# Optimization experiments

Hardware: AMD Instinct MI355X
Metric: run time of the kernel (lower is better)

Reference implementation:

```python
import jax, jax.numpy as jnp
import numpy as np

B, M, E, H, TOPK = 1024, 10000, 8, 512, 2


def setup_inputs() -> dict:
    key = jax.random.key(0)
    ks = jax.random.split(key, 6)
    s_in = 1.0 / np.sqrt(M)
    s_h = 1.0 / np.sqrt(H)
    x = jax.random.normal(ks[0], (B, M), dtype=jnp.float32)
    # Expert params, torch Linear layout stacked over experts
    W1 = jax.random.uniform(ks[1], (E, H, M), jnp.float32, -s_in, s_in)
    b1 = jax.random.uniform(ks[2], (E, H), jnp.float32, -s_in, s_in)
    W2 = jax.random.uniform(ks[3], (E, M, H), jnp.float32, -s_h, s_h)
    b2 = jax.random.uniform(ks[4], (E, M), jnp.float32, -s_h, s_h)
    Wr = jax.random.uniform(ks[5], (E, M), jnp.float32, -s_in, s_in)  # router, no bias
    return {"x": x, "W1": W1, "b1": b1, "W2": W2, "b2": b2, "Wr": Wr}


def reference(x, W1, b1, W2, b2, Wr):
    # Router: logits [B, E], sparse top-k softmax weights scattered to dense [B, E]
    logits = jnp.einsum('bm,em->be', x, Wr)
    topk_vals, topk_idx = jax.lax.top_k(logits, TOPK)
    probs = jax.nn.softmax(topk_vals, axis=-1)
    rw = jnp.zeros_like(logits).at[jnp.arange(B)[:, None], topk_idx].set(probs)
    # Dense all-expert MLP (faithful to original: every expert runs on every token)
    h = jax.nn.relu(jnp.einsum('bm,ehm->beh', x, W1) + b1)      # [B, E, H]
    eo = jnp.einsum('beh,emh->bem', h, W2) + b2                  # [B, E, M]
    # Masked weighted combine
    out = jnp.sum(rw[:, :, None] * eo, axis=1)                   # [B, M]
    return out
```

## Files before the change

### kernel.cpp

```cpp
#include <hip/hip_runtime.h>
#include <hip/hip_bf16.h>


#define B_TOK 1024
#define M_DIM 10000
#define E_NUM 8
#define H_DIM 512
#define NSTEP 313

typedef __attribute__((ext_vector_type(4))) float fx4;
typedef __attribute__((ext_vector_type(8))) short sx8;
typedef __attribute__((ext_vector_type(4))) short sx4;

#define LSTR 40

__device__ __forceinline__ short f2bf(float f) {
  union { __hip_bfloat16 h; short s; } u;
  u.h = __float2bfloat16(f);
  return u.s;
}

__device__ __forceinline__ sx8 pack8(fx4 a, fx4 b) {
  sx8 r;
  r[0] = f2bf(a[0]); r[1] = f2bf(a[1]); r[2] = f2bf(a[2]); r[3] = f2bf(a[3]);
  r[4] = f2bf(b[0]); r[5] = f2bf(b[1]); r[6] = f2bf(b[2]); r[7] = f2bf(b[3]);
  return r;
}

__global__ void k_zero(int* cnt, int* cnt2) {
  if (threadIdx.x < E_NUM) cnt[threadIdx.x] = 0;
  if (threadIdx.x < 2 * E_NUM) cnt2[threadIdx.x] = 0;
}

__global__ __launch_bounds__(256) void k_router(
    const float* __restrict__ x, const float* __restrict__ Wr,
    int* __restrict__ cnt, int* __restrict__ cnt2,
    int* __restrict__ tokAll, int* __restrict__ qlist2, float* __restrict__ wlist2)
{
  int b = blockIdx.x, t = threadIdx.x;
  const float* xr = x + (size_t)b * M_DIM;
  double acc[E_NUM];
#pragma unroll
  for (int e = 0; e < E_NUM; e++) acc[e] = 0.0;
  for (int m = t; m < M_DIM; m += 256) {
    float xv = xr[m];
#pragma unroll
    for (int e = 0; e < E_NUM; e++)
      acc[e] += (double)xv * (double)Wr[e * M_DIM + m];
  }
#pragma unroll
  for (int e = 0; e < E_NUM; e++) {
#pragma unroll
    for (int off = 32; off > 0; off >>= 1)
      acc[e] += __shfl_xor(acc[e], off);
  }
  __shared__ double part[4][E_NUM];
  int wave = t >> 6;
  if ((t & 63) == 0) {
    for (int e = 0; e < E_NUM; e++) part[wave][e] = acc[e];
  }
  __syncthreads();
  if (t == 0) {
    double lg[E_NUM];
    for (int e = 0; e < E_NUM; e++)
      lg[e] = part[0][e] + part[1][e] + part[2][e] + part[3][e];
    int i0 = 0;
    for (int e = 1; e < E_NUM; e++) if (lg[e] > lg[i0]) i0 = e;
    int i1 = (i0 == 0) ? 1 : 0;
    for (int e = 0; e < E_NUM; e++) if (e != i0 && lg[e] > lg[i1]) i1 = e;
    double ex = exp(lg[i1] - lg[i0]);
    float p0 = (float)(1.0 / (1.0 + ex));
    float p1 = (float)(ex / (1.0 + ex));
    int q0 = atomicAdd(&cnt[i0], 1);
    tokAll[i0 * B_TOK + q0] = b;
    int j0 = atomicAdd(&cnt2[i0 * 2 + 0], 1);
    qlist2[(i0 * 2 + 0) * B_TOK + j0] = q0;
    wlist2[(i0 * 2 + 0) * B_TOK + j0] = p0;
    int q1 = atomicAdd(&cnt[i1], 1);
    tokAll[i1 * B_TOK + q1] = b;
    int j1 = atomicAdd(&cnt2[i1 * 2 + 1], 1);
    qlist2[(i1 * 2 + 1) * B_TOK + j1] = q1;
    wlist2[(i1 * 2 + 1) * B_TOK + j1] = p1;
  }
}

__global__ __launch_bounds__(256) void k_mlp1(
    const float* __restrict__ x, const float* __restrict__ W1,
    const int* __restrict__ cnt, const int* __restrict__ tokAll,
    float* __restrict__ partials, int CH)
{
  int e = blockIdx.z;
  int tt = blockIdx.y >> 2, nt = blockIdx.y & 3;
  int kc = blockIdx.x;

  __shared__ int sh_ne, sh_eoff;
  __shared__ __align__(16) short As[128 * LSTR];
  __shared__ __align__(16) short Bs[128 * LSTR];
  __shared__ int toks[128];

  int t = threadIdx.x;
  if (t == 0) {
    int off = 0;
    for (int k = 0; k < e; k++) off += cnt[k];
    sh_eoff = off; sh_ne = cnt[e];
  }
  __syncthreads();
  int ne = sh_ne, eoff = sh_eoff, row0 = tt * 128;
  if (row0 >= ne) return;
  int nvalid = min(128, ne - row0);

  if (t < 128) toks[t] = tokAll[e * B_TOK + row0 + min(t, nvalid - 1)];
  __syncthreads();

  int r4 = t >> 2, kch = t & 3;
  const float* xr0 = x + (size_t)toks[r4] * M_DIM + kch * 8;
  const float* xr1 = x + (size_t)toks[r4 + 64] * M_DIM + kch * 8;
  const float* wr0 = W1 + ((size_t)e * H_DIM + nt * 128 + r4) * M_DIM + kch * 8;
  const float* wr1 = W1 + ((size_t)e * H_DIM + nt * 128 + r4 + 64) * M_DIM + kch * 8;

  int lane = t & 63, wave = t >> 6;
  int wr = wave >> 1, wc = wave & 1;
  int lrow = lane & 15, khalf = lane >> 4;

  fx4 z4 = {0.f, 0.f, 0.f, 0.f};
  fx4 acc[4][4];
#pragma unroll
  for (int m = 0; m < 4; m++)
#pragma unroll
    for (int n = 0; n < 4; n++) acc[m][n] = z4;

  int s0 = kc * CH, s1 = min(s0 + CH, NSTEP);
  sx8 zv = {0, 0, 0, 0, 0, 0, 0, 0};

  sx8 a0, a1, b0, b1v;
  {
    int k0 = s0 * 32 + kch * 8;
    bool ok = (k0 + 8 <= M_DIM);
    a0  = ok ? pack8(*(const fx4*)(xr0 + s0 * 32), *(const fx4*)(xr0 + s0 * 32 + 4)) : zv;
    a1  = ok ? pack8(*(const fx4*)(xr1 + s0 * 32), *(const fx4*)(xr1 + s0 * 32 + 4)) : zv;
    b0  = ok ? pack8(*(const fx4*)(wr0 + s0 * 32), *(const fx4*)(wr0 + s0 * 32 + 4)) : zv;
    b1v = ok ? pack8(*(const fx4*)(wr1 + s0 * 32), *(const fx4*)(wr1 + s0 * 32 + 4)) : zv;
  }

  for (int s = s0; s < s1; s++) {
    __syncthreads();
    *(sx8*)(&As[r4 * LSTR + kch * 8]) = a0;
    *(sx8*)(&As[(r4 + 64) * LSTR + kch * 8]) = a1;
    *(sx8*)(&Bs[r4 * LSTR + kch * 8]) = b0;
    *(sx8*)(&Bs[(r4 + 64) * LSTR + kch * 8]) = b1v;
    __syncthreads();
    if (s + 1 < s1) {
      int kn = (s + 1) * 32;
      bool ok = (kn + kch * 8 + 8 <= M_DIM);
      a0  = ok ? pack8(*(const fx4*)(xr0 + kn), *(const fx4*)(xr0 + kn + 4)) : zv;
      a1  = ok ? pack8(*(const fx4*)(xr1 + kn), *(const fx4*)(xr1 + kn + 4)) : zv;
      b0  = ok ? pack8(*(const fx4*)(wr0 + kn), *(const fx4*)(wr0 + kn + 4)) : zv;
      b1v = ok ? pack8(*(const fx4*)(wr1 + kn), *(const fx4*)(wr1 + kn + 4)) : zv;
    }
    sx8 af[4], bf[4];
#pragma unroll
    for (int m = 0; m < 4; m++)
      af[m] = *(const sx8*)(&As[(wr * 64 + m * 16 + lrow) * LSTR + khalf * 8]);
#pragma unroll
    for (int n = 0; n < 4; n++)
      bf[n] = *(const sx8*)(&Bs[(wc * 64 + n * 16 + lrow) * LSTR + khalf * 8]);
#pragma unroll
    for (int m = 0; m < 4; m++)
#pragma unroll
      for (int n = 0; n < 4; n++)
        acc[m][n] = __builtin_amdgcn_mfma_f32_16x16x32_bf16(af[m], bf[n], acc[m][n], 0, 0, 0);
  }

#pragma unroll
  for (int m = 0; m < 4; m++)
#pragma unroll
    for (int n = 0; n < 4; n++) {
      int colg = nt * 128 + wc * 64 + n * 16 + lrow;
#pragma unroll
      for (int r = 0; r < 4; r++) {
        int rl = wr * 64 + m * 16 + khalf * 4 + r;
        if (rl < nvalid) {
          int grow = eoff + row0 + rl;
          partials[((size_t)kc * 2048 + grow) * H_DIM + colg] = acc[m][n][r];
        }
      }
    }
}

__global__ __launch_bounds__(256) void k_hreduce(
    const float* __restrict__ partials, const float* __restrict__ b1,
    const int* __restrict__ cnt, short* __restrict__ hbuf, int KC)
{
  __shared__ int sc[E_NUM];
  int t = threadIdx.x;
  if (t < E_NUM) sc[t] = cnt[t];
  __syncthreads();
  int i = (blockIdx.x * 256 + t) * 4;
  int slot = i >> 9;
  int e = 0, off = 0;
  for (int k = 0; k < E_NUM - 1; k++) {
    if (slot >= off + sc[k]) { off += sc[k]; e++; } else break;
  }
  fx4 v = *(const fx4*)(partials + i);
  for (int kc = 1; kc < KC; kc++)
    v += *(const fx4*)(partials + (size_t)kc * 2048 * H_DIM + i);
  fx4 bv = *(const fx4*)(b1 + e * H_DIM + (i & (H_DIM - 1)));
  sx4 o;
#pragma unroll
  for (int j = 0; j < 4; j++) o[j] = f2bf(fmaxf(v[j] + bv[j], 0.f));
  *(sx4*)(hbuf + i) = o;
}

__global__ __launch_bounds__(256) void k_mlp2(
    const short* __restrict__ hbuf, const float* __restrict__ W2,
    const float* __restrict__ b2, const int* __restrict__ cnt,
    const int* __restrict__ cnt2, const int* __restrict__ tokAll,
    const int* __restrict__ qlist2, const float* __restrict__ wlist2,
    float* __restrict__ out, int ord)
{
  int e = blockIdx.z, mt = blockIdx.y, tt = blockIdx.x;

  __shared__ int sh_ne2, sh_eoff;
  __shared__ __align__(16) short As[128 * LSTR];
  __shared__ __align__(16) short Bs[128 * LSTR];
  __shared__ int sl[128];
  __shared__ int tok2[128];
  __shared__ float wts[128];

  int t = threadIdx.x;
  if (t == 0) {
    int off = 0;
    for (int k = 0; k < e; k++) off += cnt[k];
    sh_eoff = off; sh_ne2 = cnt2[e * 2 + ord];
  }
  __syncthreads();
  int ne2 = sh_ne2, eoff = sh_eoff, row0 = tt * 128;
  if (row0 >= ne2) return;
  int nvalid = min(128, ne2 - row0);

  if (t < 128) {
    int j = row0 + min(t, nvalid - 1);
    int q = qlist2[(e * 2 + ord) * B_TOK + j];
    sl[t] = eoff + q;
    tok2[t] = tokAll[e * B_TOK + q];
    wts[t] = (t < nvalid) ? wlist2[(e * 2 + ord) * B_TOK + j] : 0.f;
  }
  __syncthreads();

  int r4 = t >> 2, kch = t & 3;
  const short* hr0 = hbuf + (size_t)sl[r4] * H_DIM + kch * 8;
  const short* hr1 = hbuf + (size_t)sl[r4 + 64] * H_DIM + kch * 8;
  const float* w20 = W2 + ((size_t)e * M_DIM + min(mt * 128 + r4, M_DIM - 1)) * H_DIM + kch * 8;
  const float* w21 = W2 + ((size_t)e * M_DIM + min(mt * 128 + r4 + 64, M_DIM - 1)) * H_DIM + kch * 8;

  int lane = t & 63, wave = t >> 6;
  int wr = wave >> 1, wc = wave & 1;
  int lrow = lane & 15, khalf = lane >> 4;

  fx4 z4 = {0.f, 0.f, 0.f, 0.f};
  fx4 acc[4][4];
#pragma unroll
  for (int m = 0; m < 4; m++)
#pragma unroll
    for (int n = 0; n < 4; n++) acc[m][n] = z4;

  sx8 a0, a1, b0, b1v;
  a0  = *(const sx8*)(hr0);
  a1  = *(const sx8*)(hr1);
  b0  = pack8(*(const fx4*)(w20), *(const fx4*)(w20 + 4));
  b1v = pack8(*(const fx4*)(w21), *(const fx4*)(w21 + 4));

  for (int s = 0; s < 16; s++) {
    __syncthreads();
    *(sx8*)(&As[r4 * LSTR + kch * 8]) = a0;
    *(sx8*)(&As[(r4 + 64) * LSTR + kch * 8]) = a1;
    *(sx8*)(&Bs[r4 * LSTR + kch * 8]) = b0;
    *(sx8*)(&Bs[(r4 + 64) * LSTR + kch * 8]) = b1v;
    __syncthreads();
    if (s + 1 < 16) {
      int kn = (s + 1) * 32;
      a0  = *(const sx8*)(hr0 + kn);
      a1  = *(const sx8*)(hr1 + kn);
      b0  = pack8(*(const fx4*)(w20 + kn), *(const fx4*)(w20 + kn + 4));
      b1v = pack8(*(const fx4*)(w21 + kn), *(const fx4*)(w21 + kn + 4));
    }
    sx8 af[4], bf[4];
#pragma unroll
    for (int m = 0; m < 4; m++)
      af[m] = *(const sx8*)(&As[(wr * 64 + m * 16 + lrow) * LSTR + khalf * 8]);
#pragma unroll
    for (int n = 0; n < 4; n++)
      bf[n] = *(const sx8*)(&Bs[(wc * 64 + n * 16 + lrow) * LSTR + khalf * 8]);
#pragma unroll
    for (int m = 0; m < 4; m++)
#pragma unroll
      for (int n = 0; n < 4; n++)
        acc[m][n] = __builtin_amdgcn_mfma_f32_16x16x32_bf16(af[m], bf[n], acc[m][n], 0, 0, 0);
  }

#pragma unroll
  for (int m = 0; m < 4; m++)
#pragma unroll
    for (int n = 0; n < 4; n++) {
      int colg = mt * 128 + wc * 64 + n * 16 + lrow;
      if (colg < M_DIM) {
        float b2v = b2[(size_t)e * M_DIM + colg];
#pragma unroll
        for (int r = 0; r < 4; r++) {
          int rl = wr * 64 + m * 16 + khalf * 4 + r;
          if (rl < nvalid) {
            float v = wts[rl] * (acc[m][n][r] + b2v);
            float* dst = out + (size_t)tok2[rl] * M_DIM + colg;
            if (ord == 0) *dst = v;
            else *dst += v;
          }
        }
      }
    }
}

extern "C" void kernel_launch(void* const* d_in, const int* in_sizes, int n_in,
                              void* d_out, int out_size, void* d_ws, size_t ws_size,
                              hipStream_t stream) {
  const float* x  = (const float*)d_in[0];
  const float* W1 = (const float*)d_in[1];
  const float* b1 = (const float*)d_in[2];
  const float* W2 = (const float*)d_in[3];
  const float* b2 = (const float*)d_in[4];
  const float* Wr = (const float*)d_in[5];
  float* out = (float*)d_out;

  int KC = (ws_size >= (size_t)36 * 1024 * 1024) ? 8 : 4;
  int CH = (NSTEP + KC - 1) / KC;

  char* p = (char*)d_ws;
  float* partials = (float*)p;               p += (size_t)KC * 2048 * H_DIM * 4;
  short* hbuf     = (short*)p;               p += (size_t)2048 * H_DIM * 2;
  int*   cnt      = (int*)p;                 p += 64;
  int*   cnt2     = (int*)p;                 p += 64;
  int*   tokAll   = (int*)p;                 p += E_NUM * B_TOK * 4;
  int*   qlist2   = (int*)p;                 p += 2 * E_NUM * B_TOK * 4;
  float* wlist2   = (float*)p;

  k_zero<<<1, 64, 0, stream>>>(cnt, cnt2);
  k_router<<<B_TOK, 256, 0, stream>>>(x, Wr, cnt, cnt2, tokAll, qlist2, wlist2);
  k_mlp1<<<dim3(KC, 12, E_NUM), 256, 0, stream>>>(x, W1, cnt, tokAll, partials, CH);
  k_hreduce<<<1024, 256, 0, stream>>>(partials, b1, cnt, hbuf, KC);
  k_mlp2<<<dim3(2, 79, E_NUM), 256, 0, stream>>>(hbuf, W2, b2, cnt, cnt2, tokAll,
                                                 qlist2, wlist2, out, 0);
  k_mlp2<<<dim3(2, 79, E_NUM), 256, 0, stream>>>(hbuf, W2, b2, cnt, cnt2, tokAll,
                                                 qlist2, wlist2, out, 1);
}
```

Measured before the change: 384.5 us.

## Double-buffer LDS tiles and prefetch two steps ahead in both MLP GEMMs

Both expert GEMM kernels now use two LDS buffers with a single barrier per K-step and keep two sets of global loads in flight (prefetching steps s+2 and s+3 in alternating register sets). The bf16 conversion and LDS store for the next step happen after the MFMAs of the current step, so global latency is hidden better. A lightweight barrier waits only on LDS counters rather than a full __syncthreads. It costs double the LDS and more registers, which may lower occupancy.

```diff
diff --git a/kernel.cpp b/kernel.cpp
--- a/kernel.cpp
+++ b/kernel.cpp
@@ -13,6 +13,7 @@
 typedef __attribute__((ext_vector_type(4))) short sx4;
 
 #define LSTR 40
+#define BUFS (256 * LSTR)
 
 __device__ __forceinline__ short f2bf(float f) {
   union { __hip_bfloat16 h; short s; } u;
@@ -25,6 +26,13 @@
   r[0] = f2bf(a[0]); r[1] = f2bf(a[1]); r[2] = f2bf(a[2]); r[3] = f2bf(a[3]);
   r[4] = f2bf(b[0]); r[5] = f2bf(b[1]); r[6] = f2bf(b[2]); r[7] = f2bf(b[3]);
   return r;
+}
+
+__device__ __forceinline__ void pipe_barrier() {
+  asm volatile("s_waitcnt lgkmcnt(0)" ::: "memory");
+  __builtin_amdgcn_sched_barrier(0);
+  __builtin_amdgcn_s_barrier();
+  __builtin_amdgcn_sched_barrier(0);
 }
 
 __global__ void k_zero(int* cnt, int* cnt2) {
@@ -84,6 +92,22 @@
   }
 }
 
+#define M_MFMA(bo)                                                          \
+  do {                                                                      \
+    sx8 af[4], bfr[4];                                                      \
+    _Pragma("unroll")                                                       \
+    for (int m_ = 0; m_ < 4; m_++)                                          \
+      af[m_] = *(const sx8*)(&SB[(bo) + (wr * 64 + m_ * 16 + lrow) * LSTR + khalf * 8]); \
+    _Pragma("unroll")                                                       \
+    for (int n_ = 0; n_ < 4; n_++)                                          \
+      bfr[n_] = *(const sx8*)(&SB[(bo) + (128 + wc * 64 + n_ * 16 + lrow) * LSTR + khalf * 8]); \
+    _Pragma("unroll")                                                       \
+    for (int m_ = 0; m_ < 4; m_++)                                          \
+      _Pragma("unroll")                                                     \
+      for (int n_ = 0; n_ < 4; n_++)                                        \
+        acc[m_][n_] = __builtin_amdgcn_mfma_f32_16x16x32_bf16(af[m_], bfr[n_], acc[m_][n_], 0, 0, 0); \
+  } while (0)
+
 __global__ __launch_bounds__(256) void k_mlp1(
     const float* __restrict__ x, const float* __restrict__ W1,
     const int* __restrict__ cnt, const int* __restrict__ tokAll,
@@ -94,8 +118,7 @@
   int kc = blockIdx.x;
 
   __shared__ int sh_ne, sh_eoff;
-  __shared__ __align__(16) short As[128 * LSTR];
-  __shared__ __align__(16) short Bs[128 * LSTR];
+  __shared__ __align__(16) short SB[2 * BUFS];
   __shared__ int toks[128];
 
   int t = threadIdx.x;
@@ -113,10 +136,10 @@
   __syncthreads();
 
   int r4 = t >> 2, kch = t & 3;
-  const float* xr0 = x + (size_t)toks[r4] * M_DIM + kch * 8;
-  const float* xr1 = x + (size_t)toks[r4 + 64] * M_DIM + kch * 8;
-  const float* wr0 = W1 + ((size_t)e * H_DIM + nt * 128 + r4) * M_DIM + kch * 8;
-  const float* wr1 = W1 + ((size_t)e * H_DIM + nt * 128 + r4 + 64) * M_DIM + kch * 8;
+  const float* xr0 = x + (size_t)toks[r4] * M_DIM;
+  const float* xr1 = x + (size_t)toks[r4 + 64] * M_DIM;
+  const float* wr0 = W1 + ((size_t)e * H_DIM + nt * 128 + r4) * M_DIM;
+  const float* wr1 = W1 + ((size_t)e * H_DIM + nt * 128 + r4 + 64) * M_DIM;
 
   int lane = t & 63, wave = t >> 6;
   int wr = wave >> 1, wc = wave & 1;
@@ -132,43 +155,51 @@
   int s0 = kc * CH, s1 = min(s0 + CH, NSTEP);
   sx8 zv = {0, 0, 0, 0, 0, 0, 0, 0};
 
-  sx8 a0, a1, b0, b1v;
-  {
-    int k0 = s0 * 32 + kch * 8;
-    bool ok = (k0 + 8 <= M_DIM);
-    a0  = ok ? pack8(*(const fx4*)(xr0 + s0 * 32), *(const fx4*)(xr0 + s0 * 32 + 4)) : zv;
-    a1  = ok ? pack8(*(const fx4*)(xr1 + s0 * 32), *(const fx4*)(xr1 + s0 * 32 + 4)) : zv;
-    b0  = ok ? pack8(*(const fx4*)(wr0 + s0 * 32), *(const fx4*)(wr0 + s0 * 32 + 4)) : zv;
-    b1v = ok ? pack8(*(const fx4*)(wr1 + s0 * 32), *(const fx4*)(wr1 + s0 * 32 + 4)) : zv;
-  }
-
-  for (int s = s0; s < s1; s++) {
-    __syncthreads();
-    *(sx8*)(&As[r4 * LSTR + kch * 8]) = a0;
-    *(sx8*)(&As[(r4 + 64) * LSTR + kch * 8]) = a1;
-    *(sx8*)(&Bs[r4 * LSTR + kch * 8]) = b0;
-    *(sx8*)(&Bs[(r4 + 64) * LSTR + kch * 8]) = b1v;
-    __syncthreads();
-    if (s + 1 < s1) {
-      int kn = (s + 1) * 32;
-      bool ok = (kn + kch * 8 + 8 <= M_DIM);
-      a0  = ok ? pack8(*(const fx4*)(xr0 + kn), *(const fx4*)(xr0 + kn + 4)) : zv;
-      a1  = ok ? pack8(*(const fx4*)(xr1 + kn), *(const fx4*)(xr1 + kn + 4)) : zv;
-      b0  = ok ? pack8(*(const fx4*)(wr0 + kn), *(const fx4*)(wr0 + kn + 4)) : zv;
-      b1v = ok ? pack8(*(const fx4*)(wr1 + kn), *(const fx4*)(wr1 + kn + 4)) : zv;
-    }
-    sx8 af[4], bf[4];
-#pragma unroll
-    for (int m = 0; m < 4; m++)
-      af[m] = *(const sx8*)(&As[(wr * 64 + m * 16 + lrow) * LSTR + khalf * 8]);
-#pragma unroll
-    for (int n = 0; n < 4; n++)
-      bf[n] = *(const sx8*)(&Bs[(wc * 64 + n * 16 + lrow) * LSTR + khalf * 8]);
-#pragma unroll
-    for (int m = 0; m < 4; m++)
-#pragma unroll
-      for (int n = 0; n < 4; n++)
-        acc[m][n] = __builtin_amdgcn_mfma_f32_16x16x32_bf16(af[m], bf[n], acc[m][n], 0, 0, 0);
+#define M1_LOAD(p, sN)                                                       \
+  do {                                                                       \
+    int off_ = (sN) * 32 + kch * 8;                                          \
+    int oc_ = min(off_, M_DIM - 8);                                          \
+    p##ok = (off_ + 8 <= M_DIM);                                             \
+    p##A0 = *(const fx4*)(xr0 + oc_); p##A0b = *(const fx4*)(xr0 + oc_ + 4); \
+    p##A1 = *(const fx4*)(xr1 + oc_); p##A1b = *(const fx4*)(xr1 + oc_ + 4); \
+    p##B0 = *(const fx4*)(wr0 + oc_); p##B0b = *(const fx4*)(wr0 + oc_ + 4); \
+    p##B1 = *(const fx4*)(wr1 + oc_); p##B1b = *(const fx4*)(wr1 + oc_ + 4); \
+  } while (0)
+
+#define M1_PACK(p, wo)                                                       \
+  do {                                                                       \
+    sx8 t0_ = p##ok ? pack8(p##A0, p##A0b) : zv;                             \
+    sx8 t1_ = p##ok ? pack8(p##A1, p##A1b) : zv;                             \
+    sx8 t2_ = p##ok ? pack8(p##B0, p##B0b) : zv;                             \
+    sx8 t3_ = p##ok ? pack8(p##B1, p##B1b) : zv;                             \
+    *(sx8*)(&SB[(wo) + r4 * LSTR + kch * 8]) = t0_;                          \
+    *(sx8*)(&SB[(wo) + (r4 + 64) * LSTR + kch * 8]) = t1_;                   \
+    *(sx8*)(&SB[(wo) + (128 + r4) * LSTR + kch * 8]) = t2_;                  \
+    *(sx8*)(&SB[(wo) + (128 + r4 + 64) * LSTR + kch * 8]) = t3_;             \
+  } while (0)
+
+  fx4 pA0, pA0b, pA1, pA1b, pB0, pB0b, pB1, pB1b; bool pok;
+  fx4 qA0, qA0b, qA1, qA1b, qB0, qB0b, qB1, qB1b; bool qok;
+
+  M1_LOAD(p, s0);
+  M1_PACK(p, 0);
+  M1_LOAD(p, s0 + 1);
+  M1_LOAD(q, s0 + 2);
+  pipe_barrier();
+
+  int c = 0, s = s0;
+  while (s < s1) {
+    M_MFMA(c * BUFS);
+    if (s + 1 < s1) M1_PACK(p, (c ^ 1) * BUFS);
+    if (s + 3 < s1) M1_LOAD(p, s + 3);
+    pipe_barrier();
+    c ^= 1; s++;
+    if (s >= s1) break;
+    M_MFMA(c * BUFS);
+    if (s + 1 < s1) M1_PACK(q, (c ^ 1) * BUFS);
+    if (s + 3 < s1) M1_LOAD(q, s + 3);
+    pipe_barrier();
+    c ^= 1; s++;
   }
 
 #pragma unroll
@@ -185,6 +216,8 @@
         }
       }
     }
+#undef M1_LOAD
+#undef M1_PACK
 }
 
 __global__ __launch_bounds__(256) void k_hreduce(
@@ -221,8 +254,7 @@
   int e = blockIdx.z, mt = blockIdx.y, tt = blockIdx.x;
 
   __shared__ int sh_ne2, sh_eoff;
-  __shared__ __align__(16) short As[128 * LSTR];
-  __shared__ __align__(16) short Bs[128 * LSTR];
+  __shared__ __align__(16) short SB[2 * BUFS];
   __shared__ int sl[128];
   __shared__ int tok2[128];
   __shared__ float wts[128];
@@ -248,10 +280,10 @@
   __syncthreads();
 
   int r4 = t >> 2, kch = t & 3;
-  const short* hr0 = hbuf + (size_t)sl[r4] * H_DIM + kch * 8;
-  const short* hr1 = hbuf + (size_t)sl[r4 + 64] * H_DIM + kch * 8;
-  const float* w20 = W2 + ((size_t)e * M_DIM + min(mt * 128 + r4, M_DIM - 1)) * H_DIM + kch * 8;
-  const float* w21 = W2 + ((size_t)e * M_DIM + min(mt * 128 + r4 + 64, M_DIM - 1)) * H_DIM + kch * 8;
+  const short* hr0 = hbuf + (size_t)sl[r4] * H_DIM;
+  const short* hr1 = hbuf + (size_t)sl[r4 + 64] * H_DIM;
+  const float* w20 = W2 + ((size_t)e * M_DIM + min(mt * 128 + r4, M_DIM - 1)) * H_DIM;
+  const float* w21 = W2 + ((size_t)e * M_DIM + min(mt * 128 + r4 + 64, M_DIM - 1)) * H_DIM;
 
   int lane = t & 63, wave = t >> 6;
   int wr = wave >> 1, wc = wave & 1;
@@ -264,38 +296,47 @@
 #pragma unroll
     for (int n = 0; n < 4; n++) acc[m][n] = z4;
 
-  sx8 a0, a1, b0, b1v;
-  a0  = *(const sx8*)(hr0);
-  a1  = *(const sx8*)(hr1);
-  b0  = pack8(*(const fx4*)(w20), *(const fx4*)(w20 + 4));
-  b1v = pack8(*(const fx4*)(w21), *(const fx4*)(w21 + 4));
-
-  for (int s = 0; s < 16; s++) {
-    __syncthreads();
-    *(sx8*)(&As[r4 * LSTR + kch * 8]) = a0;
-    *(sx8*)(&As[(r4 + 64) * LSTR + kch * 8]) = a1;
-    *(sx8*)(&Bs[r4 * LSTR + kch * 8]) = b0;
-    *(sx8*)(&Bs[(r4 + 64) * LSTR + kch * 8]) = b1v;
-    __syncthreads();
-    if (s + 1 < 16) {
-      int kn = (s + 1) * 32;
-      a0  = *(const sx8*)(hr0 + kn);
-      a1  = *(const sx8*)(hr1 + kn);
-      b0  = pack8(*(const fx4*)(w20 + kn), *(const fx4*)(w20 + kn + 4));
-      b1v = pack8(*(const fx4*)(w21 + kn), *(const fx4*)(w21 + kn + 4));
-    }
-    sx8 af[4], bf[4];
-#pragma unroll
-    for (int m = 0; m < 4; m++)
-      af[m] = *(const sx8*)(&As[(wr * 64 + m * 16 + lrow) * LSTR + khalf * 8]);
-#pragma unroll
-    for (int n = 0; n < 4; n++)
-      bf[n] = *(const sx8*)(&Bs[(wc * 64 + n * 16 + lrow) * LSTR + khalf * 8]);
-#pragma unroll
-    for (int m = 0; m < 4; m++)
-#pragma unroll
-      for (int n = 0; n < 4; n++)
-        acc[m][n] = __builtin_amdgcn_mfma_f32_16x16x32_bf16(af[m], bf[n], acc[m][n], 0, 0, 0);
+#define M2_LOAD(p, sN)                                                       \
+  do {                                                                       \
+    int off_ = (sN) * 32 + kch * 8;                                          \
+    p##As0 = *(const sx8*)(hr0 + off_);                                      \
+    p##As1 = *(const sx8*)(hr1 + off_);                                      \
+    p##B0 = *(const fx4*)(w20 + off_); p##B0b = *(const fx4*)(w20 + off_ + 4); \
+    p##B1 = *(const fx4*)(w21 + off_); p##B1b = *(const fx4*)(w21 + off_ + 4); \
+  } while (0)
+
+#define M2_PACK(p, wo)                                                       \
+  do {                                                                       \
+    sx8 t2_ = pack8(p##B0, p##B0b);                                          \
+    sx8 t3_ = pack8(p##B1, p##B1b);                                          \
+    *(sx8*)(&SB[(wo) + r4 * LSTR + kch * 8]) = p##As0;                       \
+    *(sx8*)(&SB[(wo) + (r4 + 64) * LSTR + kch * 8]) = p##As1;                \
+    *(sx8*)(&SB[(wo) + (128 + r4) * LSTR + kch * 8]) = t2_;                  \
+    *(sx8*)(&SB[(wo) + (128 + r4 + 64) * LSTR + kch * 8]) = t3_;             \
+  } while (0)
+
+  sx8 pAs0, pAs1; fx4 pB0, pB0b, pB1, pB1b;
+  sx8 qAs0, qAs1; fx4 qB0, qB0b, qB1, qB1b;
+
+  M2_LOAD(p, 0);
+  M2_PACK(p, 0);
+  M2_LOAD(p, 1);
+  M2_LOAD(q, 2);
+  pipe_barrier();
+
+  int c = 0, s = 0;
+  while (s < 16) {
+    M_MFMA(c * BUFS);
+    if (s + 1 < 16) M2_PACK(p, (c ^ 1) * BUFS);
+    if (s + 3 < 16) M2_LOAD(p, s + 3);
+    pipe_barrier();
+    c ^= 1; s++;
+    if (s >= 16) break;
+    M_MFMA(c * BUFS);
+    if (s + 1 < 16) M2_PACK(q, (c ^ 1) * BUFS);
+    if (s + 3 < 16) M2_LOAD(q, s + 3);
+    pipe_barrier();
+    c ^= 1; s++;
   }
 
 #pragma unroll
@@ -317,6 +358,8 @@
         }
       }
     }
+#undef M2_LOAD
+#undef M2_PACK
 }
 
 extern "C" void kernel_launch(void* const* d_in, const int* in_sizes, int n_in,
@@ -334,12 +377,12 @@
   int CH = (NSTEP + KC - 1) / KC;
 
   char* p = (char*)d_ws;
-  float* partials = (float*)p;               p += (size_t)KC * 2048 * H_DIM * 4;
-  short* hbuf     = (short*)p;               p += (size_t)2048 * H_DIM * 2;
-  int*   cnt      = (int*)p;                 p += 64;
-  int*   cnt2     = (int*)p;                 p += 64;
-  int*   tokAll   = (int*)p;                 p += E_NUM * B_TOK * 4;
-  int*   qlist2   = (int*)p;                 p += 2 * E_NUM * B_TOK * 4;
+  float* partials = (float*)p;        p += (size_t)KC * 2048 * H_DIM * 4;
+  short* hbuf     = (short*)p;        p += (size_t)2048 * H_DIM * 2;
+  int*   cnt      = (int*)p;          p += 64;
+  int*   cnt2     = (int*)p;          p += 64;
+  int*   tokAll   = (int*)p;          p += E_NUM * B_TOK * 4;
+  int*   qlist2   = (int*)p;          p += 2 * E_NUM * B_TOK * 4;
   float* wlist2   = (float*)p;
 
   k_zero<<<1, 64, 0, stream>>>(cnt, cnt2);
```

Result: slower. 431.2 us (+12.1%).
